# Kernel optimization log

Hardware: AMD Instinct MI355X
Metric: run time of the kernel (lower is better)

The kernel has to match this reference:

```python
import jax, jax.numpy as jnp
import numpy as np


def setup_inputs() -> dict:
    key = jax.random.key(0)
    k1, k2 = jax.random.split(key)
    B, L, E, K = 4, 1024, 512, 8
    xsa = jax.random.normal(k1, (B, L, E), dtype=jnp.float32)
    # attq.weight, torch Linear layout (out_features=K*E, in_features=E); scaled like a trained init
    Wq = jax.random.normal(k2, (K * E, E), dtype=jnp.float32) * 0.02
    return {"xsa": xsa, "Wq": Wq}


def reference(xsa, Wq):
    # xsa: (B, L, E); Wq: (K*E, E). attq bias, attk, and bias layers are unused in the original forward.
    B, L, E = xsa.shape
    K = Wq.shape[0] // E
    q = (xsa @ Wq.T).reshape(B, L, K, E)            # (B, L, K, E)
    # hijk = q @ xsa^T over E, per batch: (B, L, K, L)
    hijk = jnp.einsum('blke,bme->blkm', q, xsa) * (1.0 / (E ** 0.5))
    pijk = jax.nn.softmax(hijk, axis=-1)            # (B, L, K, L)
    yik = jnp.einsum('blkm,bme->blke', pijk, xsa)   # (B, L, K, E)  xsa doubles as V
    xid = yik.reshape(B, L, K * E)
    return (xid, pijk)
```

## Files before the change

kernel.cpp:

```cpp
#include <hip/hip_runtime.h>
#include <cstdint>
#include <cstddef>


typedef __bf16 bf16x8 __attribute__((ext_vector_type(8)));
typedef float f32x4 __attribute__((ext_vector_type(4)));

#define BM 128
#define BN 128
#define BK 64

__device__ __forceinline__ unsigned short f2bf(float f) {
  union { float f; unsigned int u; } x; x.f = f;
  unsigned int u = x.u;
  unsigned int r = (u + 0x7fffu + ((u >> 16) & 1u)) >> 16;
  return (unsigned short)r;
}

__device__ __forceinline__ void async_cp16(const void* g, void* l) {
  __builtin_amdgcn_global_load_lds(
      (const __attribute__((address_space(1))) void*)g,
      (__attribute__((address_space(3))) void*)l, 16, 0, 0);
}

template <bool A_F32, bool OUT_BF16>
__global__ __launch_bounds__(256) void gemm_nt(
    const void* __restrict__ Av, const unsigned short* __restrict__ Bt,
    void* __restrict__ Cv, int M, int N, int Kd,
    size_t sA, size_t sB, size_t sC, float scale) {
  __shared__ __align__(16) unsigned char smem[BM * BK * 2 + BN * BK * 2];
  unsigned short* As = (unsigned short*)smem;
  unsigned short* Bs = (unsigned short*)(smem + BM * BK * 2);

  const int tid  = threadIdx.x;
  const int lane = tid & 63;
  const int wave = tid >> 6;
  const int wm   = (wave >> 1) * 64;
  const int wn   = (wave & 1) * 64;
  const int quad = lane >> 4;
  const int lrow = lane & 15;

  const int m0 = blockIdx.x * BM;
  const int n0 = blockIdx.y * BN;
  const int b  = blockIdx.z;

  const unsigned short* Bb = Bt + (size_t)b * sB;

  const int arow = lane >> 3;
  const int agcb = (lane & 7) ^ arow;

  const int srow = tid >> 3;
  const int scb  = tid & 7;

  f32x4 acc[4][4];
#pragma unroll
  for (int i = 0; i < 4; ++i)
#pragma unroll
    for (int j = 0; j < 4; ++j) acc[i][j] = (f32x4){0.f, 0.f, 0.f, 0.f};

  for (int k0 = 0; k0 < Kd; k0 += BK) {
    float4 pf[4][2];
    if constexpr (A_F32) {
      const float* Ab = (const float*)Av + (size_t)b * sA;
#pragma unroll
      for (int j = 0; j < 4; ++j) {
        int row = j * 32 + srow;
        const float* src = Ab + (size_t)(m0 + row) * Kd + k0 + scb * 8;
        pf[j][0] = *(const float4*)(src);
        pf[j][1] = *(const float4*)(src + 4);
      }
    }
    __syncthreads();
    if constexpr (!A_F32) {
      const unsigned short* Ab = (const unsigned short*)Av + (size_t)b * sA;
#pragma unroll
      for (int t = 0; t < 4; ++t) {
        int c = wave * 4 + t;
        async_cp16(Ab + (size_t)(m0 + c * 8 + arow) * Kd + k0 + agcb * 8,
                   As + c * 512);
      }
    } else {
#pragma unroll
      for (int j = 0; j < 4; ++j) {
        int row = j * 32 + srow;
        union { unsigned short s[8]; uint4 v; } pk;
        pk.s[0] = f2bf(pf[j][0].x); pk.s[1] = f2bf(pf[j][0].y);
        pk.s[2] = f2bf(pf[j][0].z); pk.s[3] = f2bf(pf[j][0].w);
        pk.s[4] = f2bf(pf[j][1].x); pk.s[5] = f2bf(pf[j][1].y);
        pk.s[6] = f2bf(pf[j][1].z); pk.s[7] = f2bf(pf[j][1].w);
        *(uint4*)&As[row * 64 + ((scb ^ (row & 7)) << 3)] = pk.v;
      }
    }
#pragma unroll
    for (int t = 0; t < 4; ++t) {
      int c = wave * 4 + t;
      async_cp16(Bb + (size_t)(n0 + c * 8 + arow) * Kd + k0 + agcb * 8,
                 Bs + c * 512);
    }
    __syncthreads();
#pragma unroll
    for (int ks = 0; ks < BK; ks += 32) {
      bf16x8 af[4], bfr[4];
#pragma unroll
      for (int i = 0; i < 4; ++i) {
        int r = wm + i * 16 + lrow;
        int cb = (ks >> 3) + quad;
        af[i] = *(const bf16x8*)&As[r * 64 + ((cb ^ (r & 7)) << 3)];
      }
#pragma unroll
      for (int j = 0; j < 4; ++j) {
        int r = wn + j * 16 + lrow;
        int cb = (ks >> 3) + quad;
        bfr[j] = *(const bf16x8*)&Bs[r * 64 + ((cb ^ (r & 7)) << 3)];
      }
#pragma unroll
      for (int i = 0; i < 4; ++i)
#pragma unroll
        for (int j = 0; j < 4; ++j)
          acc[i][j] = __builtin_amdgcn_mfma_f32_16x16x32_bf16(af[i], bfr[j], acc[i][j], 0, 0, 0);
    }
  }

  __syncthreads();
  float* epi = (float*)smem;
  const int erow = (wm ? 16 : 0) + quad * 4;
#pragma unroll
  for (int i = 0; i < 4; ++i) {
#pragma unroll
    for (int j = 0; j < 4; ++j)
#pragma unroll
      for (int r = 0; r < 4; ++r)
        epi[(erow + r) * 132 + wn + j * 16 + lrow] = acc[i][j][r] * scale;
    __syncthreads();
    if constexpr (OUT_BF16) {
      unsigned short* C = (unsigned short*)Cv + (size_t)b * sC;
      int trow = tid >> 4, tcol = (tid & 15) * 8;
#pragma unroll
      for (int rep = 0; rep < 2; ++rep) {
        int lr = trow + rep * 16;
        int grow = m0 + i * 16 + lr + (lr >= 16 ? 48 : 0);
        union { unsigned short s[8]; uint4 v; } pk;
#pragma unroll
        for (int u = 0; u < 8; ++u) pk.s[u] = f2bf(epi[lr * 132 + tcol + u]);
        *(uint4*)&C[(size_t)grow * N + n0 + tcol] = pk.v;
      }
    } else {
      float* C = (float*)Cv + (size_t)b * sC;
      int trow = tid >> 5, tcol = (tid & 31) * 4;
#pragma unroll
      for (int rep = 0; rep < 4; ++rep) {
        int lr = trow + rep * 8;
        int grow = m0 + i * 16 + lr + (lr >= 16 ? 48 : 0);
        *(float4*)&C[(size_t)grow * N + n0 + tcol] = *(const float4*)&epi[lr * 132 + tcol];
      }
    }
    __syncthreads();
  }
}

__global__ __launch_bounds__(256) void cvt_f32_to_bf16(
    const float* __restrict__ in, unsigned short* __restrict__ out, int n4) {
  int i = blockIdx.x * blockDim.x + threadIdx.x;
  if (i < n4) {
    float4 v = *(const float4*)(in + (size_t)i * 4);
    union { unsigned short s[4]; uint2 v2; } pk;
    pk.s[0] = f2bf(v.x); pk.s[1] = f2bf(v.y);
    pk.s[2] = f2bf(v.z); pk.s[3] = f2bf(v.w);
    *(uint2*)(out + (size_t)i * 4) = pk.v2;
  }
}

__global__ __launch_bounds__(256) void transpose_to_bf16(
    const float* __restrict__ in, unsigned short* __restrict__ out, int L, int E) {
  __shared__ unsigned short tile[32][33];
  int b  = blockIdx.z;
  int e0 = blockIdx.x * 32;
  int l0 = blockIdx.y * 32;
  int tx = threadIdx.x & 31;
  int ty = threadIdx.x >> 5;
  const float* inb = in + (size_t)b * L * E;
#pragma unroll
  for (int r = 0; r < 32; r += 8)
    tile[ty + r][tx] = f2bf(inb[(size_t)(l0 + ty + r) * E + e0 + tx]);
  __syncthreads();
  unsigned short* outb = out + (size_t)b * L * E;
#pragma unroll
  for (int r = 0; r < 32; r += 8)
    outb[(size_t)(e0 + ty + r) * L + l0 + tx] = tile[tx][ty + r];
}

__global__ __launch_bounds__(256) void softmax_rows(float* __restrict__ p, int ncol) {
  size_t row = blockIdx.x;
  float* pr = p + row * (size_t)ncol;
  int tid = threadIdx.x;
  float4 v = *(const float4*)(pr + tid * 4);
  float m = fmaxf(fmaxf(v.x, v.y), fmaxf(v.z, v.w));
#pragma unroll
  for (int off = 1; off < 64; off <<= 1) m = fmaxf(m, __shfl_xor(m, off));
  __shared__ float redm[4];
  __shared__ float reds[4];
  int w = tid >> 6;
  if ((tid & 63) == 0) redm[w] = m;
  __syncthreads();
  m = fmaxf(fmaxf(redm[0], redm[1]), fmaxf(redm[2], redm[3]));
  float e0 = __expf(v.x - m);
  float e1 = __expf(v.y - m);
  float e2 = __expf(v.z - m);
  float e3 = __expf(v.w - m);
  float s = e0 + e1 + e2 + e3;
#pragma unroll
  for (int off = 1; off < 64; off <<= 1) s += __shfl_xor(s, off);
  if ((tid & 63) == 0) reds[w] = s;
  __syncthreads();
  s = reds[0] + reds[1] + reds[2] + reds[3];
  float inv = 1.0f / s;
  float4 o = make_float4(e0 * inv, e1 * inv, e2 * inv, e3 * inv);
  *(float4*)(pr + tid * 4) = o;
}

extern "C" void kernel_launch(void* const* d_in, const int* in_sizes, int n_in,
                              void* d_out, int out_size, void* d_ws, size_t ws_size,
                              hipStream_t stream) {
  const float* xsa = (const float*)d_in[0];
  const float* Wq  = (const float*)d_in[1];
  float* out = (float*)d_out;

  const int Bn = 4, L = 1024, E = 512, K = 8;
  const int M1 = Bn * L;
  const int N1 = K * E;
  const size_t xid_n = (size_t)Bn * L * K * E;

  float* xid  = out;
  float* pijk = out + xid_n;

  unsigned short* ws   = (unsigned short*)d_ws;
  unsigned short* WqB  = ws;
  unsigned short* xsaB = WqB + (size_t)N1 * E;
  unsigned short* xsaT = xsaB + (size_t)Bn * L * E;
  unsigned short* QB   = xsaT + (size_t)Bn * L * E;

  {
    int n4 = (N1 * E) / 4;
    cvt_f32_to_bf16<<<dim3((n4 + 255) / 256), dim3(256), 0, stream>>>(Wq, WqB, n4);
    int m4 = (Bn * L * E) / 4;
    cvt_f32_to_bf16<<<dim3((m4 + 255) / 256), dim3(256), 0, stream>>>(xsa, xsaB, m4);
    transpose_to_bf16<<<dim3(E / 32, L / 32, Bn), dim3(256), 0, stream>>>(xsa, xsaT, L, E);
  }

  gemm_nt<false, true><<<dim3(M1 / BM, N1 / BN, 1), dim3(256), 0, stream>>>(
      xsaB, WqB, QB, M1, N1, E, 0, 0, 0, 1.0f);

  gemm_nt<false, false><<<dim3((L * K) / BM, L / BN, Bn), dim3(256), 0, stream>>>(
      QB, xsaB, pijk, L * K, L, E,
      (size_t)L * K * E, (size_t)L * E, (size_t)L * K * L, 0.04419417382415922f);

  softmax_rows<<<dim3(Bn * L * K), dim3(256), 0, stream>>>(pijk, L);

  gemm_nt<true, false><<<dim3((L * K) / BM, E / BN, Bn), dim3(256), 0, stream>>>(
      pijk, xsaT, xid, L * K, E, L,
      (size_t)L * K * L, (size_t)E * L, (size_t)L * K * E, 1.0f);
}
```

Before: 361.1 us.

## Fuse exp and row-sum into score GEMM, store bf16 unnormalized probabilities

The score GEMM now applies exp(scale*x) in its epilogue, writes unnormalized probabilities as bf16, and accumulates row sums with atomics. A light normalize kernel then writes the fp32 pijk output, and the PV GEMM reads bf16 probabilities through async LDS loads, applying 1/sum in its epilogue. This removes the separate softmax read-modify-write pass and the fp32 A-operand load and convert in the last GEMM. In exchange it skips max subtraction, which risks overflow for large logits, and adds atomic contention plus an extra memset.

```diff
diff --git a/kernel.cpp b/kernel.cpp
--- a/kernel.cpp
+++ b/kernel.cpp
@@ -17,17 +17,22 @@
   return (unsigned short)r;
 }
 
+__device__ __forceinline__ float bf2f(unsigned short s) {
+  union { unsigned int u; float f; } x; x.u = ((unsigned int)s) << 16;
+  return x.f;
+}
+
 __device__ __forceinline__ void async_cp16(const void* g, void* l) {
   __builtin_amdgcn_global_load_lds(
       (const __attribute__((address_space(1))) void*)g,
       (__attribute__((address_space(3))) void*)l, 16, 0, 0);
 }
 
-template <bool A_F32, bool OUT_BF16>
+template <int MODE>
 __global__ __launch_bounds__(256) void gemm_nt(
-    const void* __restrict__ Av, const unsigned short* __restrict__ Bt,
-    void* __restrict__ Cv, int M, int N, int Kd,
-    size_t sA, size_t sB, size_t sC, float scale) {
+    const unsigned short* __restrict__ A, const unsigned short* __restrict__ Bt,
+    void* __restrict__ Cv, float* __restrict__ sums,
+    int M, int N, int Kd, size_t sA, size_t sB, size_t sC, float scale) {
   __shared__ __align__(16) unsigned char smem[BM * BK * 2 + BN * BK * 2];
   unsigned short* As = (unsigned short*)smem;
   unsigned short* Bs = (unsigned short*)(smem + BM * BK * 2);
@@ -44,14 +49,12 @@
   const int n0 = blockIdx.y * BN;
   const int b  = blockIdx.z;
 
+  const unsigned short* Ab = A + (size_t)b * sA;
   const unsigned short* Bb = Bt + (size_t)b * sB;
 
   const int arow = lane >> 3;
   const int agcb = (lane & 7) ^ arow;
 
-  const int srow = tid >> 3;
-  const int scb  = tid & 7;
-
   f32x4 acc[4][4];
 #pragma unroll
   for (int i = 0; i < 4; ++i)
@@ -59,37 +62,12 @@
     for (int j = 0; j < 4; ++j) acc[i][j] = (f32x4){0.f, 0.f, 0.f, 0.f};
 
   for (int k0 = 0; k0 < Kd; k0 += BK) {
-    float4 pf[4][2];
-    if constexpr (A_F32) {
-      const float* Ab = (const float*)Av + (size_t)b * sA;
-#pragma unroll
-      for (int j = 0; j < 4; ++j) {
-        int row = j * 32 + srow;
-        const float* src = Ab + (size_t)(m0 + row) * Kd + k0 + scb * 8;
-        pf[j][0] = *(const float4*)(src);
-        pf[j][1] = *(const float4*)(src + 4);
-      }
-    }
-    __syncthreads();
-    if constexpr (!A_F32) {
-      const unsigned short* Ab = (const unsigned short*)Av + (size_t)b * sA;
-#pragma unroll
-      for (int t = 0; t < 4; ++t) {
-        int c = wave * 4 + t;
-        async_cp16(Ab + (size_t)(m0 + c * 8 + arow) * Kd + k0 + agcb * 8,
-                   As + c * 512);
-      }
-    } else {
-#pragma unroll
-      for (int j = 0; j < 4; ++j) {
-        int row = j * 32 + srow;
-        union { unsigned short s[8]; uint4 v; } pk;
-        pk.s[0] = f2bf(pf[j][0].x); pk.s[1] = f2bf(pf[j][0].y);
-        pk.s[2] = f2bf(pf[j][0].z); pk.s[3] = f2bf(pf[j][0].w);
-        pk.s[4] = f2bf(pf[j][1].x); pk.s[5] = f2bf(pf[j][1].y);
-        pk.s[6] = f2bf(pf[j][1].z); pk.s[7] = f2bf(pf[j][1].w);
-        *(uint4*)&As[row * 64 + ((scb ^ (row & 7)) << 3)] = pk.v;
-      }
+    __syncthreads();
+#pragma unroll
+    for (int t = 0; t < 4; ++t) {
+      int c = wave * 4 + t;
+      async_cp16(Ab + (size_t)(m0 + c * 8 + arow) * Kd + k0 + agcb * 8,
+                 As + c * 512);
     }
 #pragma unroll
     for (int t = 0; t < 4; ++t) {
@@ -121,6 +99,14 @@
     }
   }
 
+  float linv[4][4];
+  if constexpr (MODE == 2) {
+#pragma unroll
+    for (int i = 0; i < 4; ++i)
+#pragma unroll
+      for (int r = 0; r < 4; ++r)
+        linv[i][r] = 1.0f / sums[(size_t)b * M + m0 + wm + i * 16 + quad * 4 + r];
+  }
   __syncthreads();
   float* epi = (float*)smem;
   const int erow = (wm ? 16 : 0) + quad * 4;
@@ -129,20 +115,39 @@
 #pragma unroll
     for (int j = 0; j < 4; ++j)
 #pragma unroll
-      for (int r = 0; r < 4; ++r)
-        epi[(erow + r) * 132 + wn + j * 16 + lrow] = acc[i][j][r] * scale;
-    __syncthreads();
-    if constexpr (OUT_BF16) {
+      for (int r = 0; r < 4; ++r) {
+        float v = acc[i][j][r];
+        if constexpr (MODE == 0) v *= scale;
+        if constexpr (MODE == 1) v = __expf(v * scale);
+        if constexpr (MODE == 2) v *= linv[i][r];
+        epi[(erow + r) * 132 + wn + j * 16 + lrow] = v;
+      }
+    __syncthreads();
+    if constexpr (MODE <= 1) {
       unsigned short* C = (unsigned short*)Cv + (size_t)b * sC;
       int trow = tid >> 4, tcol = (tid & 15) * 8;
 #pragma unroll
       for (int rep = 0; rep < 2; ++rep) {
         int lr = trow + rep * 16;
         int grow = m0 + i * 16 + lr + (lr >= 16 ? 48 : 0);
+        float vals[8];
+#pragma unroll
+        for (int u = 0; u < 8; ++u) vals[u] = epi[lr * 132 + tcol + u];
         union { unsigned short s[8]; uint4 v; } pk;
 #pragma unroll
-        for (int u = 0; u < 8; ++u) pk.s[u] = f2bf(epi[lr * 132 + tcol + u]);
+        for (int u = 0; u < 8; ++u) pk.s[u] = f2bf(vals[u]);
         *(uint4*)&C[(size_t)grow * N + n0 + tcol] = pk.v;
+        if constexpr (MODE == 1) {
+          float s = 0.f;
+#pragma unroll
+          for (int u = 0; u < 8; ++u) s += vals[u];
+          s += __shfl_xor(s, 1);
+          s += __shfl_xor(s, 2);
+          s += __shfl_xor(s, 4);
+          s += __shfl_xor(s, 8);
+          if ((tid & 15) == 0)
+            atomicAdd(&sums[(size_t)b * M + grow], s);
+        }
       }
     } else {
       float* C = (float*)Cv + (size_t)b * sC;
@@ -189,33 +194,19 @@
     outb[(size_t)(e0 + ty + r) * L + l0 + tx] = tile[tx][ty + r];
 }
 
-__global__ __launch_bounds__(256) void softmax_rows(float* __restrict__ p, int ncol) {
+__global__ __launch_bounds__(256) void normalize_rows(
+    const unsigned short* __restrict__ Pu, const float* __restrict__ sums,
+    float* __restrict__ P) {
   size_t row = blockIdx.x;
-  float* pr = p + row * (size_t)ncol;
-  int tid = threadIdx.x;
-  float4 v = *(const float4*)(pr + tid * 4);
-  float m = fmaxf(fmaxf(v.x, v.y), fmaxf(v.z, v.w));
-#pragma unroll
-  for (int off = 1; off < 64; off <<= 1) m = fmaxf(m, __shfl_xor(m, off));
-  __shared__ float redm[4];
-  __shared__ float reds[4];
-  int w = tid >> 6;
-  if ((tid & 63) == 0) redm[w] = m;
-  __syncthreads();
-  m = fmaxf(fmaxf(redm[0], redm[1]), fmaxf(redm[2], redm[3]));
-  float e0 = __expf(v.x - m);
-  float e1 = __expf(v.y - m);
-  float e2 = __expf(v.z - m);
-  float e3 = __expf(v.w - m);
-  float s = e0 + e1 + e2 + e3;
-#pragma unroll
-  for (int off = 1; off < 64; off <<= 1) s += __shfl_xor(s, off);
-  if ((tid & 63) == 0) reds[w] = s;
-  __syncthreads();
-  s = reds[0] + reds[1] + reds[2] + reds[3];
-  float inv = 1.0f / s;
-  float4 o = make_float4(e0 * inv, e1 * inv, e2 * inv, e3 * inv);
-  *(float4*)(pr + tid * 4) = o;
+  int t = threadIdx.x;
+  float inv = 1.0f / sums[row];
+  uint2 u = *(const uint2*)(Pu + row * 1024 + t * 4);
+  float4 o;
+  o.x = bf2f((unsigned short)(u.x & 0xffff)) * inv;
+  o.y = bf2f((unsigned short)(u.x >> 16)) * inv;
+  o.z = bf2f((unsigned short)(u.y & 0xffff)) * inv;
+  o.w = bf2f((unsigned short)(u.y >> 16)) * inv;
+  *(float4*)(P + row * 1024 + t * 4) = o;
 }
 
 extern "C" void kernel_launch(void* const* d_in, const int* in_sizes, int n_in,
@@ -228,6 +219,7 @@
   const int Bn = 4, L = 1024, E = 512, K = 8;
   const int M1 = Bn * L;
   const int N1 = K * E;
+  const int M2 = L * K;
   const size_t xid_n = (size_t)Bn * L * K * E;
 
   float* xid  = out;
@@ -238,6 +230,8 @@
   unsigned short* xsaB = WqB + (size_t)N1 * E;
   unsigned short* xsaT = xsaB + (size_t)Bn * L * E;
   unsigned short* QB   = xsaT + (size_t)Bn * L * E;
+  unsigned short* PuB  = QB + (size_t)M1 * N1;
+  float* sums = (float*)(PuB + (size_t)Bn * M2 * L);
 
   {
     int n4 = (N1 * E) / 4;
@@ -245,18 +239,19 @@
     int m4 = (Bn * L * E) / 4;
     cvt_f32_to_bf16<<<dim3((m4 + 255) / 256), dim3(256), 0, stream>>>(xsa, xsaB, m4);
     transpose_to_bf16<<<dim3(E / 32, L / 32, Bn), dim3(256), 0, stream>>>(xsa, xsaT, L, E);
-  }
-
-  gemm_nt<false, true><<<dim3(M1 / BM, N1 / BN, 1), dim3(256), 0, stream>>>(
-      xsaB, WqB, QB, M1, N1, E, 0, 0, 0, 1.0f);
-
-  gemm_nt<false, false><<<dim3((L * K) / BM, L / BN, Bn), dim3(256), 0, stream>>>(
-      QB, xsaB, pijk, L * K, L, E,
-      (size_t)L * K * E, (size_t)L * E, (size_t)L * K * L, 0.04419417382415922f);
-
-  softmax_rows<<<dim3(Bn * L * K), dim3(256), 0, stream>>>(pijk, L);
-
-  gemm_nt<true, false><<<dim3((L * K) / BM, E / BN, Bn), dim3(256), 0, stream>>>(
-      pijk, xsaT, xid, L * K, E, L,
-      (size_t)L * K * L, (size_t)E * L, (size_t)L * K * E, 1.0f);
-}
+    hipMemsetAsync(sums, 0, (size_t)Bn * M2 * sizeof(float), stream);
+  }
+
+  gemm_nt<0><<<dim3(M1 / BM, N1 / BN, 1), dim3(256), 0, stream>>>(
+      xsaB, WqB, QB, nullptr, M1, N1, E, 0, 0, 0, 1.0f);
+
+  gemm_nt<1><<<dim3(M2 / BM, L / BN, Bn), dim3(256), 0, stream>>>(
+      QB, xsaB, PuB, sums, M2, L, E,
+      (size_t)M2 * E, (size_t)L * E, (size_t)M2 * L, 0.04419417382415922f);
+
+  normalize_rows<<<dim3(Bn * M2), dim3(256), 0, stream>>>(PuB, sums, pijk);
+
+  gemm_nt<2><<<dim3(M2 / BM, E / BN, Bn), dim3(256), 0, stream>>>(
+      PuB, xsaT, xid, sums, M2, E, L,
+      (size_t)M2 * L, (size_t)E * L, (size_t)M2 * E, 1.0f);
+}
```

Result: faster. 353.0 us (-2.2%).
